# Optimization experiments

Hardware: AMD Instinct MI355X
Metric: run time of the kernel (lower is better)

## Reference

```python
import jax, jax.numpy as jnp
import numpy as np

CLIP = 50.0
EPS = 1e-8


def _attn_jacobian_agg(q, k, v, scale):
    """Aggregate attention Jacobian dO/dq summed over queries, plus attention outputs.

    q: (B, Q, d); k, v: (B, S, d).
    Per-query Jacobian: J_q = scale * sum_j p_j v_j (k_j - kbar)^T, kbar = sum_i p_i k_i.
    Returns (agg_jac: (B, d, d), outputs: (B, Q, d)).
    """
    scores = jnp.einsum('bqd,bsd->bqs', q, k) * scale
    p = jax.nn.softmax(scores, axis=-1)
    out = jnp.einsum('bqs,bsd->bqd', p, v)           # attention outputs O
    kbar = jnp.einsum('bqs,bsd->bqd', p, k)          # expected key per query
    # sum_j p_j v_j k_j^T  -> (B, Q, d, d)
    pvk = jnp.einsum('bqs,bsd,bse->bqde', p, v, k)
    jac = scale * (pvk - out[..., :, None] * kbar[..., None, :])
    return jac.sum(axis=1), out


def setup_inputs() -> dict:
    key = jax.random.key(0)
    ks = jax.random.split(key, 5)
    B, Q, S, M, D = 256, 16, 512, 8, 128
    return {
        'queries': jax.random.normal(ks[0], (B, Q, D), dtype=jnp.float32),
        'keys':    jax.random.normal(ks[1], (B, S, D), dtype=jnp.float32),
        'values':  jax.random.normal(ks[2], (B, S, D), dtype=jnp.float32),
        'k_cg':    jax.random.normal(ks[3], (B, M, D), dtype=jnp.float32),
        'v_cg':    jax.random.normal(ks[4], (B, M, D), dtype=jnp.float32),
    }


def reference(queries, keys, values, k_cg, v_cg):
    B, Q, d = queries.shape
    scale = d ** -0.5

    dense_jac, dense_out = _attn_jacobian_agg(queries, keys, values, scale)
    cg_jac, cg_out = _attn_jacobian_agg(queries, k_cg, v_cg, scale)

    # jacobian_clip_value = 50.0 (config default)
    dense_jac = jnp.clip(dense_jac, -CLIP, CLIP)
    cg_jac = jnp.clip(cg_jac, -CLIP, CLIP)

    df = dense_jac.reshape(B, -1)
    cf = cg_jac.reshape(B, -1)
    dn = jnp.linalg.norm(df, axis=-1)
    cn = jnp.linalg.norm(cf, axis=-1)
    cosine_sim = (df * cf).sum(axis=-1) / (dn * cn + EPS)
    force_direction_loss = 1.0 - cosine_sim

    # consistency: per-query output MSE, averaged over queries, scaled by 1/d_head
    out_diff = dense_out - cg_out
    per_query_mse = (out_diff ** 2).sum(axis=-1)          # (B, Q)
    consistency_loss = per_query_mse.sum(axis=-1) / Q / d  # (B,)

    # v4 loss: L = w_dir * L_force_cos + w_cons * L_consistency (defaults 1.0, 1.0)
    total = 1.0 * force_direction_loss + 1.0 * consistency_loss
    return total.mean()  # reduction='mean'
```

## Files before the change

kernel.cpp:

```cpp
#include <hip/hip_runtime.h>
#include <math.h>


namespace {
constexpr int Bn = 256, Qn = 16, Sn = 512, Mn = 8, Dn = 128;
constexpr int NT = 512;
constexpr float SCALE = 0.08838834764831845f;
constexpr float CLIPV = 50.0f;

constexpr int QS   = 0;
constexpr int PB   = 4352;
constexpr int WOFF = 20992;
constexpr int SMX0 = 23040;
constexpr int SMX1 = 23552;
constexpr int KT   = 24064;
constexpr int VT   = 34304;
constexpr int VTW  = 39424;
constexpr int CGS  = 44544;
constexpr int PCG  = 45056;
constexpr int WC   = 46336;
constexpr int RED  = 46368;
constexpr int LDSZ = 46496;

typedef __attribute__((ext_vector_type(8))) short bf16x8;
typedef __attribute__((ext_vector_type(4))) float f32x4;
#define MFMA16(a, b, c) __builtin_amdgcn_mfma_f32_16x16x32_bf16((a), (b), (c), 0, 0, 0)

__device__ inline unsigned int pack2t(float a, float b) {
  return __builtin_amdgcn_perm(__builtin_bit_cast(unsigned int, b),
                               __builtin_bit_cast(unsigned int, a), 0x07060302u);
}
__device__ inline unsigned short f2bf(float x) {
  unsigned int u = __builtin_bit_cast(unsigned int, x);
  u += 0x7fffu + ((u >> 16) & 1u);
  return (unsigned short)(u >> 16);
}
__device__ inline float bf2f(unsigned short h) {
  unsigned int u = ((unsigned int)h) << 16;
  return __builtin_bit_cast(float, u);
}
union Frag {
  bf16x8 v;
  unsigned int u[4];
  unsigned short h[8];
};

__global__ void zero_ws_kernel(float4* ws) {
  ws[threadIdx.x] = make_float4(0.f, 0.f, 0.f, 0.f);
}

__global__ void finalize_kernel(const float* __restrict__ ws, float* __restrict__ out) {
  __shared__ float sr[256];
  int i = threadIdx.x;
  float dt = ws[i * 4 + 0], n1 = ws[i * 4 + 1], n2 = ws[i * 4 + 2], cs = ws[i * 4 + 3];
  float cosv = dt / (sqrtf(n1) * sqrtf(n2) + 1e-8f);
  sr[i] = (1.0f - cosv) + cs * (1.0f / (float)(Qn * Dn));
  __syncthreads();
  for (int off = 128; off; off >>= 1) {
    if (i < off) sr[i] += sr[i + off];
    __syncthreads();
  }
  if (i == 0) out[0] = sr[0] * (1.0f / (float)Bn);
}

__global__ __launch_bounds__(NT, 6) void fm_kernel(
    const float* __restrict__ Qg, const float* __restrict__ Kg,
    const float* __restrict__ Vg, const float* __restrict__ Kcg,
    const float* __restrict__ Vcg, float* __restrict__ ws) {
  __shared__ __align__(16) char L[LDSZ];
  const int bid = blockIdx.x, b = bid >> 1, h = bid & 1;
  const int t = threadIdx.x, lane = t & 63, wv = t >> 6;
  const int quad = lane >> 4, l16 = lane & 15;

  const float* Qb = Qg + (size_t)b * Qn * Dn;
  const float* Kb = Kg + (size_t)b * Sn * Dn;
  const float* Vb = Vg + (size_t)b * Sn * Dn;
  const float* Kc = Kcg + (size_t)b * Mn * Dn;
  const float* Vc = Vcg + (size_t)b * Mn * Dn;

  const int dK = t & 127, gK = t >> 7;
  const int dV = t & 63, gV = (t >> 6) & 3;
  const bool vrole = t < 256;
  float kpf[8], vpf[8];

  auto load_tiles = [&](int st) {
    int s0 = st * 32 + gK * 8;
#pragma unroll
    for (int i = 0; i < 8; ++i) kpf[i] = Kb[(size_t)(s0 + i) * Dn + dK];
    if (vrole) {
      int s1 = st * 32 + gV * 8;
#pragma unroll
      for (int i = 0; i < 8; ++i) vpf[i] = Vb[(size_t)(s1 + i) * Dn + h * 64 + dV];
    }
  };
  auto store_tiles = [&](int st) {
    unsigned int u0 = pack2t(kpf[0], kpf[1]), u1 = pack2t(kpf[2], kpf[3]);
    unsigned int u2 = pack2t(kpf[4], kpf[5]), u3 = pack2t(kpf[6], kpf[7]);
    *(uint4*)(L + KT + dK * 80 + gK * 16) = make_uint4(u0, u1, u2, u3);
    if (vrole) {
      int s1 = st * 32 + gV * 8;
      float4 wlo = *(const float4*)(L + WOFF + s1 * 4);
      float4 whi = *(const float4*)(L + WOFF + s1 * 4 + 16);
      float wv8[8] = {wlo.x, wlo.y, wlo.z, wlo.w, whi.x, whi.y, whi.z, whi.w};
      unsigned int v0 = pack2t(vpf[0], vpf[1]), v1 = pack2t(vpf[2], vpf[3]);
      unsigned int v2 = pack2t(vpf[4], vpf[5]), v3 = pack2t(vpf[6], vpf[7]);
      *(uint4*)(L + VT + dV * 80 + gV * 16) = make_uint4(v0, v1, v2, v3);
      unsigned int w0 = pack2t(wv8[0] * vpf[0], wv8[1] * vpf[1]);
      unsigned int w1 = pack2t(wv8[2] * vpf[2], wv8[3] * vpf[3]);
      unsigned int w2 = pack2t(wv8[4] * vpf[4], wv8[5] * vpf[5]);
      unsigned int w3 = pack2t(wv8[6] * vpf[6], wv8[7] * vpf[7]);
      *(uint4*)(L + VTW + dV * 80 + gV * 16) = make_uint4(w0, w1, w2, w3);
    }
  };

  {
    int row = t >> 5, c4 = t & 31;
    float4 qv = ((const float4*)Qb)[t];
    unsigned int p0 = pack2t(qv.x * SCALE, qv.y * SCALE);
    unsigned int p1 = pack2t(qv.z * SCALE, qv.w * SCALE);
    *(unsigned long long*)(L + QS + row * 272 + c4 * 8) =
        (unsigned long long)p0 | ((unsigned long long)p1 << 32);
  }
  __syncthreads();

  float sc[4][4];
  {
    bf16x8 aq[4];
#pragma unroll
    for (int kk = 0; kk < 4; ++kk)
      aq[kk] = *(const bf16x8*)(L + QS + l16 * 272 + kk * 64 + quad * 16);
#pragma unroll
    for (int j = 0; j < 4; ++j) {
      const float* kp = Kb + (size_t)(64 * wv + 16 * j + l16) * Dn + quad * 8;
      f32x4 acc = {0.f, 0.f, 0.f, 0.f};
#pragma unroll
      for (int kk = 0; kk < 4; ++kk) {
        float4 lo = *(const float4*)(kp + kk * 32);
        float4 hi = *(const float4*)(kp + kk * 32 + 4);
        Frag f;
        f.u[0] = pack2t(lo.x, lo.y);
        f.u[1] = pack2t(lo.z, lo.w);
        f.u[2] = pack2t(hi.x, hi.y);
        f.u[3] = pack2t(hi.z, hi.w);
        acc = MFMA16(aq[kk], f.v, acc);
      }
#pragma unroll
      for (int r = 0; r < 4; ++r) sc[j][r] = acc[r];
    }
  }
  load_tiles(0);

  {
    float pm[4];
#pragma unroll
    for (int r = 0; r < 4; ++r)
      pm[r] = fmaxf(fmaxf(sc[0][r], sc[1][r]), fmaxf(sc[2][r], sc[3][r]));
#pragma unroll
    for (int o = 8; o; o >>= 1) {
#pragma unroll
      for (int r = 0; r < 4; ++r) pm[r] = fmaxf(pm[r], __shfl_xor(pm[r], o));
    }
    if (l16 == 0) {
#pragma unroll
      for (int r = 0; r < 4; ++r)
        *(float*)(L + SMX0 + ((quad * 4 + r) * 8 + wv) * 4) = pm[r];
    }
    __syncthreads();
    float gm[4];
#pragma unroll
    for (int r = 0; r < 4; ++r) {
      int q = quad * 4 + r;
      float4 a = *(const float4*)(L + SMX0 + q * 32);
      float4 c = *(const float4*)(L + SMX0 + q * 32 + 16);
      gm[r] = fmaxf(fmaxf(fmaxf(a.x, a.y), fmaxf(a.z, a.w)),
                    fmaxf(fmaxf(c.x, c.y), fmaxf(c.z, c.w)));
    }
    float ps[4] = {0.f, 0.f, 0.f, 0.f};
#pragma unroll
    for (int j = 0; j < 4; ++j) {
#pragma unroll
      for (int r = 0; r < 4; ++r) {
        sc[j][r] = __expf(sc[j][r] - gm[r]);
        ps[r] += sc[j][r];
      }
    }
#pragma unroll
    for (int o = 8; o; o >>= 1) {
#pragma unroll
      for (int r = 0; r < 4; ++r) ps[r] += __shfl_xor(ps[r], o);
    }
    if (l16 == 0) {
#pragma unroll
      for (int r = 0; r < 4; ++r)
        *(float*)(L + SMX1 + ((quad * 4 + r) * 8 + wv) * 4) = ps[r];
    }
    __syncthreads();
    float inv[4];
#pragma unroll
    for (int r = 0; r < 4; ++r) {
      int q = quad * 4 + r;
      float4 a = *(const float4*)(L + SMX1 + q * 32);
      float4 c = *(const float4*)(L + SMX1 + q * 32 + 16);
      inv[r] = 1.f / (a.x + a.y + a.z + a.w + c.x + c.y + c.z + c.w);
    }
#pragma unroll
    for (int j = 0; j < 4; ++j) {
      int s = 64 * wv + 16 * j + l16;
      float wpart = 0.f;
#pragma unroll
      for (int r = 0; r < 4; ++r) {
        float p = sc[j][r] * inv[r];
        *(unsigned short*)(L + PB + (quad * 4 + r) * 1040 + s * 2) = f2bf(p);
        wpart += p;
      }
      wpart += __shfl_xor(wpart, 16);
      wpart += __shfl_xor(wpart, 32);
      if (quad == j) *(float*)(L + WOFF + s * 4) = wpart;
    }
  }
  __syncthreads();

  const int rp = wv & 1, ch = wv >> 1;
  f32x4 C00 = {0.f,0.f,0.f,0.f}, C01 = {0.f,0.f,0.f,0.f};
  f32x4 C10 = {0.f,0.f,0.f,0.f}, C11 = {0.f,0.f,0.f,0.f};
  f32x4 outacc = {0.f,0.f,0.f,0.f}, kbacc = {0.f,0.f,0.f,0.f};

  auto ckstep = [&](f32x4& c00, f32x4& c01, f32x4& c10, f32x4& c11) {
    bf16x8 A0 = *(const bf16x8*)(L + VTW + (rp * 32 + l16) * 80 + quad * 16);
    bf16x8 A1 = *(const bf16x8*)(L + VTW + (rp * 32 + 16 + l16) * 80 + quad * 16);
    bf16x8 B0 = *(const bf16x8*)(L + KT + (ch * 32 + l16) * 80 + quad * 16);
    bf16x8 B1 = *(const bf16x8*)(L + KT + (ch * 32 + 16 + l16) * 80 + quad * 16);
    c00 = MFMA16(A0, B0, c00);
    c01 = MFMA16(A0, B1, c01);
    c10 = MFMA16(A1, B0, c10);
    c11 = MFMA16(A1, B1, c11);
  };

  for (int st = 0; st < 16; ++st) {
    if (st) __syncthreads();
    store_tiles(st);
    __syncthreads();
    if (st < 15) load_tiles(st + 1);
    bf16x8 pA = *(const bf16x8*)(L + PB + l16 * 1040 + st * 64 + quad * 16);
    bf16x8 bK = *(const bf16x8*)(L + KT + (wv * 16 + l16) * 80 + quad * 16);
    kbacc = MFMA16(pA, bK, kbacc);
    if (wv < 4) {
      bf16x8 bV = *(const bf16x8*)(L + VT + (wv * 16 + l16) * 80 + quad * 16);
      outacc = MFMA16(pA, bV, outacc);
    }
    ckstep(C00, C01, C10, C11);
  }
  __syncthreads();

  if (wv < 4) {
#pragma unroll
    for (int r = 0; r < 4; ++r)
      *(unsigned short*)(L + VTW + (wv * 16 + l16) * 80 + (quad * 4 + r) * 2) = f2bf(-outacc[r]);
  }
#pragma unroll
  for (int r = 0; r < 4; ++r)
    *(unsigned short*)(L + KT + (wv * 16 + l16) * 80 + (quad * 4 + r) * 2) = f2bf(kbacc[r]);
  if (t < 256) {
    *(uint4*)(L + KT + (t >> 1) * 80 + 32 + (t & 1) * 16) = make_uint4(0, 0, 0, 0);
  } else if (t < 384) {
    int i = t - 256;
    *(uint4*)(L + VTW + (i >> 1) * 80 + 32 + (i & 1) * 16) = make_uint4(0, 0, 0, 0);
  }
  __syncthreads();
  ckstep(C00, C01, C10, C11);
#pragma unroll
  for (int r = 0; r < 4; ++r) {
    C00[r] = fminf(fmaxf(SCALE * C00[r], -CLIPV), CLIPV);
    C01[r] = fminf(fmaxf(SCALE * C01[r], -CLIPV), CLIPV);
    C10[r] = fminf(fmaxf(SCALE * C10[r], -CLIPV), CLIPV);
    C11[r] = fminf(fmaxf(SCALE * C11[r], -CLIPV), CLIPV);
  }
  __syncthreads();

  if (wv == 0) {
    f32x4 acc = {0.f, 0.f, 0.f, 0.f};
    const float* kp = Kc + (size_t)(l16 & 7) * Dn + quad * 8;
#pragma unroll
    for (int kk = 0; kk < 4; ++kk) {
      bf16x8 a = *(const bf16x8*)(L + QS + l16 * 272 + kk * 64 + quad * 16);
      float4 lo = *(const float4*)(kp + kk * 32);
      float4 hi = *(const float4*)(kp + kk * 32 + 4);
      Frag f;
      f.u[0] = pack2t(lo.x, lo.y);
      f.u[1] = pack2t(lo.z, lo.w);
      f.u[2] = pack2t(hi.x, hi.y);
      f.u[3] = pack2t(hi.z, hi.w);
      acc = MFMA16(a, f.v, acc);
    }
    if (l16 < 8) {
#pragma unroll
      for (int r = 0; r < 4; ++r)
        *(float*)(L + CGS + (quad * 4 + r) * 32 + l16 * 4) = acc[r];
    }
  }
  __syncthreads();
  if (t < 16) {
    float xs[8];
    float m = -1e30f;
#pragma unroll
    for (int s = 0; s < 8; ++s) { xs[s] = *(const float*)(L + CGS + t * 32 + s * 4); m = fmaxf(m, xs[s]); }
    float ssum = 0.f;
#pragma unroll
    for (int s = 0; s < 8; ++s) { xs[s] = __expf(xs[s] - m); ssum += xs[s]; }
    float inv = 1.f / ssum;
#pragma unroll
    for (int s = 0; s < 4; ++s)
      *(unsigned int*)(L + PCG + t * 80 + s * 4) = pack2t(xs[2 * s] * inv, xs[2 * s + 1] * inv);
#pragma unroll
    for (int p = 4; p < 16; ++p) *(unsigned int*)(L + PCG + t * 80 + p * 4) = 0u;
  }
  __syncthreads();
  if (t < 8) {
    float s = 0.f;
#pragma unroll
    for (int q = 0; q < Qn; ++q) s += bf2f(*(const unsigned short*)(L + PCG + q * 80 + t * 2));
    *(float*)(L + WC + t * 4) = s;
  }
  __syncthreads();
  if (t < 128) {
    float kv[8];
#pragma unroll
    for (int i = 0; i < 8; ++i) kv[i] = Kc[(size_t)i * Dn + t];
    *(uint4*)(L + KT + t * 80) = make_uint4(pack2t(kv[0], kv[1]), pack2t(kv[2], kv[3]),
                                            pack2t(kv[4], kv[5]), pack2t(kv[6], kv[7]));
    *(uint4*)(L + KT + t * 80 + 16) = make_uint4(0, 0, 0, 0);
    *(uint4*)(L + KT + t * 80 + 32) = make_uint4(0, 0, 0, 0);
    *(uint4*)(L + KT + t * 80 + 48) = make_uint4(0, 0, 0, 0);
  } else if (t < 192) {
    int d = t - 128;
    float vv2[8];
#pragma unroll
    for (int i = 0; i < 8; ++i) vv2[i] = Vc[(size_t)i * Dn + h * 64 + d];
    *(uint4*)(L + VT + d * 80) = make_uint4(pack2t(vv2[0], vv2[1]), pack2t(vv2[2], vv2[3]),
                                            pack2t(vv2[4], vv2[5]), pack2t(vv2[6], vv2[7]));
    *(uint4*)(L + VT + d * 80 + 16) = make_uint4(0, 0, 0, 0);
    *(uint4*)(L + VT + d * 80 + 32) = make_uint4(0, 0, 0, 0);
    *(uint4*)(L + VT + d * 80 + 48) = make_uint4(0, 0, 0, 0);
  } else if (t < 256) {
    int d = t - 192;
    float vv2[8], wcv[8];
#pragma unroll
    for (int i = 0; i < 8; ++i) {
      vv2[i] = Vc[(size_t)i * Dn + h * 64 + d];
      wcv[i] = *(const float*)(L + WC + i * 4);
    }
    *(uint4*)(L + VTW + d * 80) =
        make_uint4(pack2t(wcv[0] * vv2[0], wcv[1] * vv2[1]), pack2t(wcv[2] * vv2[2], wcv[3] * vv2[3]),
                   pack2t(wcv[4] * vv2[4], wcv[5] * vv2[5]), pack2t(wcv[6] * vv2[6], wcv[7] * vv2[7]));
    *(uint4*)(L + VTW + d * 80 + 16) = make_uint4(0, 0, 0, 0);
    *(uint4*)(L + VTW + d * 80 + 32) = make_uint4(0, 0, 0, 0);
    *(uint4*)(L + VTW + d * 80 + 48) = make_uint4(0, 0, 0, 0);
  }
  __syncthreads();
  f32x4 outc = {0.f,0.f,0.f,0.f}, kbc = {0.f,0.f,0.f,0.f};
  f32x4 D00 = {0.f,0.f,0.f,0.f}, D01 = {0.f,0.f,0.f,0.f};
  f32x4 D10 = {0.f,0.f,0.f,0.f}, D11 = {0.f,0.f,0.f,0.f};
  {
    bf16x8 pA = *(const bf16x8*)(L + PCG + l16 * 80 + quad * 16);
    bf16x8 bK = *(const bf16x8*)(L + KT + (wv * 16 + l16) * 80 + quad * 16);
    kbc = MFMA16(pA, bK, kbc);
    if (wv < 4) {
      bf16x8 bV = *(const bf16x8*)(L + VT + (wv * 16 + l16) * 80 + quad * 16);
      outc = MFMA16(pA, bV, outc);
    }
    ckstep(D00, D01, D10, D11);
  }
  __syncthreads();
  if (wv < 4) {
#pragma unroll
    for (int r = 0; r < 4; ++r)
      *(unsigned short*)(L + VTW + (wv * 16 + l16) * 80 + (quad * 4 + r) * 2) = f2bf(-outc[r]);
  }
#pragma unroll
  for (int r = 0; r < 4; ++r)
    *(unsigned short*)(L + KT + (wv * 16 + l16) * 80 + (quad * 4 + r) * 2) = f2bf(kbc[r]);
  __syncthreads();
  ckstep(D00, D01, D10, D11);
#pragma unroll
  for (int r = 0; r < 4; ++r) {
    D00[r] = fminf(fmaxf(SCALE * D00[r], -CLIPV), CLIPV);
    D01[r] = fminf(fmaxf(SCALE * D01[r], -CLIPV), CLIPV);
    D10[r] = fminf(fmaxf(SCALE * D10[r], -CLIPV), CLIPV);
    D11[r] = fminf(fmaxf(SCALE * D11[r], -CLIPV), CLIPV);
  }

  float dot = 0.f, nd2 = 0.f, nc2 = 0.f, cons = 0.f;
#pragma unroll
  for (int r = 0; r < 4; ++r) {
    dot += C00[r] * D00[r] + C01[r] * D01[r] + C10[r] * D10[r] + C11[r] * D11[r];
    nd2 += C00[r] * C00[r] + C01[r] * C01[r] + C10[r] * C10[r] + C11[r] * C11[r];
    nc2 += D00[r] * D00[r] + D01[r] * D01[r] + D10[r] * D10[r] + D11[r] * D11[r];
  }
  if (wv < 4) {
#pragma unroll
    for (int r = 0; r < 4; ++r) {
      float df = outacc[r] - outc[r];
      cons += df * df;
    }
  }
#pragma unroll
  for (int o = 32; o; o >>= 1) {
    dot += __shfl_xor(dot, o);
    nd2 += __shfl_xor(nd2, o);
    nc2 += __shfl_xor(nc2, o);
    cons += __shfl_xor(cons, o);
  }
  if (lane == 0) {
    float* red = (float*)(L + RED);
    red[wv * 4 + 0] = dot;
    red[wv * 4 + 1] = nd2;
    red[wv * 4 + 2] = nc2;
    red[wv * 4 + 3] = cons;
  }
  __syncthreads();
  if (t == 0) {
    const float* red = (const float*)(L + RED);
    float d_ = 0.f, n1 = 0.f, n2 = 0.f, cs = 0.f;
#pragma unroll
    for (int w = 0; w < 8; ++w) {
      d_ += red[w * 4 + 0];
      n1 += red[w * 4 + 1];
      n2 += red[w * 4 + 2];
      cs += red[w * 4 + 3];
    }
    atomicAdd(ws + b * 4 + 0, d_);
    atomicAdd(ws + b * 4 + 1, n1);
    atomicAdd(ws + b * 4 + 2, n2);
    atomicAdd(ws + b * 4 + 3, cs);
  }
}
}

extern "C" void kernel_launch(void* const* d_in, const int* in_sizes, int n_in,
                              void* d_out, int out_size, void* d_ws, size_t ws_size,
                              hipStream_t stream) {
  const float* q = (const float*)d_in[0];
  const float* k = (const float*)d_in[1];
  const float* v = (const float*)d_in[2];
  const float* kc = (const float*)d_in[3];
  const float* vc = (const float*)d_in[4];
  float* out = (float*)d_out;
  float* ws = (float*)d_ws;
  zero_ws_kernel<<<1, 256, 0, stream>>>((float4*)ws);
  fm_kernel<<<2 * Bn, NT, 0, stream>>>(q, k, v, kc, vc, ws);
  finalize_kernel<<<1, 256, 0, stream>>>(ws, out);
}
```

Measured before the change: 181.2 us.

## Split each batch's Jacobian across four blocks by value and key halves

Each batch is now split into four blocks instead of two, each owning one half of the value dimension and one half of the key dimension of the d×d Jacobian. Per-block K tiles shrink to 64 columns, so the LDS footprint drops and the layout is repacked, and each wave now does two MFMAs per step instead of four. Launch bounds rise to 8 blocks per CU for more occupancy. In exchange, the softmax and score computation plus the Q load are repeated in twice as many blocks, and K and V rows are read from global memory by more blocks.

```diff
diff --git a/kernel.cpp b/kernel.cpp
--- a/kernel.cpp
+++ b/kernel.cpp
@@ -14,13 +14,13 @@
 constexpr int SMX0 = 23040;
 constexpr int SMX1 = 23552;
 constexpr int KT   = 24064;
-constexpr int VT   = 34304;
-constexpr int VTW  = 39424;
-constexpr int CGS  = 44544;
-constexpr int PCG  = 45056;
-constexpr int WC   = 46336;
-constexpr int RED  = 46368;
-constexpr int LDSZ = 46496;
+constexpr int VT   = 29184;
+constexpr int VTW  = 34304;
+constexpr int LDSZ = 39424;
+constexpr int CGS  = 20992;
+constexpr int PCG  = 21504;
+constexpr int WC   = 22784;
+constexpr int RED  = 22816;
 
 typedef __attribute__((ext_vector_type(8))) short bf16x8;
 typedef __attribute__((ext_vector_type(4))) float f32x4;
@@ -63,12 +63,13 @@
   if (i == 0) out[0] = sr[0] * (1.0f / (float)Bn);
 }
 
-__global__ __launch_bounds__(NT, 6) void fm_kernel(
+__global__ __launch_bounds__(NT, 8) void fm_kernel(
     const float* __restrict__ Qg, const float* __restrict__ Kg,
     const float* __restrict__ Vg, const float* __restrict__ Kcg,
     const float* __restrict__ Vcg, float* __restrict__ ws) {
   __shared__ __align__(16) char L[LDSZ];
-  const int bid = blockIdx.x, b = bid >> 1, h = bid & 1;
+  const int bid = blockIdx.x;
+  const int b = bid >> 2, hv = bid & 1, hk = (bid >> 1) & 1;
   const int t = threadIdx.x, lane = t & 63, wv = t >> 6;
   const int quad = lane >> 4, l16 = lane & 15;
 
@@ -78,38 +79,33 @@
   const float* Kc = Kcg + (size_t)b * Mn * Dn;
   const float* Vc = Vcg + (size_t)b * Mn * Dn;
 
-  const int dK = t & 127, gK = t >> 7;
-  const int dV = t & 63, gV = (t >> 6) & 3;
-  const bool vrole = t < 256;
-  float kpf[8], vpf[8];
+  const bool kRole = t < 256;
+  const int dS = t & 63, g8 = (t >> 6) & 3;
+  float pf[8];
 
   auto load_tiles = [&](int st) {
-    int s0 = st * 32 + gK * 8;
-#pragma unroll
-    for (int i = 0; i < 8; ++i) kpf[i] = Kb[(size_t)(s0 + i) * Dn + dK];
-    if (vrole) {
-      int s1 = st * 32 + gV * 8;
-#pragma unroll
-      for (int i = 0; i < 8; ++i) vpf[i] = Vb[(size_t)(s1 + i) * Dn + h * 64 + dV];
-    }
+    int s0 = st * 32 + g8 * 8;
+    const float* base = kRole ? (Kb + (size_t)s0 * Dn + hk * 64 + dS)
+                              : (Vb + (size_t)s0 * Dn + hv * 64 + dS);
+#pragma unroll
+    for (int i = 0; i < 8; ++i) pf[i] = base[(size_t)i * Dn];
   };
   auto store_tiles = [&](int st) {
-    unsigned int u0 = pack2t(kpf[0], kpf[1]), u1 = pack2t(kpf[2], kpf[3]);
-    unsigned int u2 = pack2t(kpf[4], kpf[5]), u3 = pack2t(kpf[6], kpf[7]);
-    *(uint4*)(L + KT + dK * 80 + gK * 16) = make_uint4(u0, u1, u2, u3);
-    if (vrole) {
-      int s1 = st * 32 + gV * 8;
+    if (kRole) {
+      *(uint4*)(L + KT + dS * 80 + g8 * 16) =
+          make_uint4(pack2t(pf[0], pf[1]), pack2t(pf[2], pf[3]),
+                     pack2t(pf[4], pf[5]), pack2t(pf[6], pf[7]));
+    } else {
+      int s1 = st * 32 + g8 * 8;
       float4 wlo = *(const float4*)(L + WOFF + s1 * 4);
       float4 whi = *(const float4*)(L + WOFF + s1 * 4 + 16);
-      float wv8[8] = {wlo.x, wlo.y, wlo.z, wlo.w, whi.x, whi.y, whi.z, whi.w};
-      unsigned int v0 = pack2t(vpf[0], vpf[1]), v1 = pack2t(vpf[2], vpf[3]);
-      unsigned int v2 = pack2t(vpf[4], vpf[5]), v3 = pack2t(vpf[6], vpf[7]);
-      *(uint4*)(L + VT + dV * 80 + gV * 16) = make_uint4(v0, v1, v2, v3);
-      unsigned int w0 = pack2t(wv8[0] * vpf[0], wv8[1] * vpf[1]);
-      unsigned int w1 = pack2t(wv8[2] * vpf[2], wv8[3] * vpf[3]);
-      unsigned int w2 = pack2t(wv8[4] * vpf[4], wv8[5] * vpf[5]);
-      unsigned int w3 = pack2t(wv8[6] * vpf[6], wv8[7] * vpf[7]);
-      *(uint4*)(L + VTW + dV * 80 + gV * 16) = make_uint4(w0, w1, w2, w3);
+      float w8[8] = {wlo.x, wlo.y, wlo.z, wlo.w, whi.x, whi.y, whi.z, whi.w};
+      *(uint4*)(L + VT + dS * 80 + g8 * 16) =
+          make_uint4(pack2t(pf[0], pf[1]), pack2t(pf[2], pf[3]),
+                     pack2t(pf[4], pf[5]), pack2t(pf[6], pf[7]));
+      *(uint4*)(L + VTW + dS * 80 + g8 * 16) =
+          make_uint4(pack2t(w8[0] * pf[0], w8[1] * pf[1]), pack2t(w8[2] * pf[2], w8[3] * pf[3]),
+                     pack2t(w8[4] * pf[4], w8[5] * pf[5]), pack2t(w8[6] * pf[6], w8[7] * pf[7]));
     }
   };
 
@@ -220,20 +216,17 @@
   }
   __syncthreads();
 
-  const int rp = wv & 1, ch = wv >> 1;
-  f32x4 C00 = {0.f,0.f,0.f,0.f}, C01 = {0.f,0.f,0.f,0.f};
-  f32x4 C10 = {0.f,0.f,0.f,0.f}, C11 = {0.f,0.f,0.f,0.f};
-  f32x4 outacc = {0.f,0.f,0.f,0.f}, kbacc = {0.f,0.f,0.f,0.f};
-
-  auto ckstep = [&](f32x4& c00, f32x4& c01, f32x4& c10, f32x4& c11) {
-    bf16x8 A0 = *(const bf16x8*)(L + VTW + (rp * 32 + l16) * 80 + quad * 16);
-    bf16x8 A1 = *(const bf16x8*)(L + VTW + (rp * 32 + 16 + l16) * 80 + quad * 16);
-    bf16x8 B0 = *(const bf16x8*)(L + KT + (ch * 32 + l16) * 80 + quad * 16);
-    bf16x8 B1 = *(const bf16x8*)(L + KT + (ch * 32 + 16 + l16) * 80 + quad * 16);
-    c00 = MFMA16(A0, B0, c00);
-    c01 = MFMA16(A0, B1, c01);
-    c10 = MFMA16(A1, B0, c10);
-    c11 = MFMA16(A1, B1, c11);
+  const int rp = wv & 3, chn = wv >> 2;
+  f32x4 c0 = {0.f,0.f,0.f,0.f}, c1 = {0.f,0.f,0.f,0.f};
+  f32x4 okacc = {0.f,0.f,0.f,0.f};
+  const char* okBase = (wv < 4) ? (L + VT) : (L + KT);
+
+  auto ckstep = [&](f32x4& a0, f32x4& a1) {
+    bf16x8 A0 = *(const bf16x8*)(L + VTW + (rp * 16 + l16) * 80 + quad * 16);
+    bf16x8 B0 = *(const bf16x8*)(L + KT + (chn * 32 + l16) * 80 + quad * 16);
+    bf16x8 B1 = *(const bf16x8*)(L + KT + (chn * 32 + 16 + l16) * 80 + quad * 16);
+    a0 = MFMA16(A0, B0, a0);
+    a1 = MFMA16(A0, B1, a1);
   };
 
   for (int st = 0; st < 16; ++st) {
@@ -242,38 +235,33 @@
     __syncthreads();
     if (st < 15) load_tiles(st + 1);
     bf16x8 pA = *(const bf16x8*)(L + PB + l16 * 1040 + st * 64 + quad * 16);
-    bf16x8 bK = *(const bf16x8*)(L + KT + (wv * 16 + l16) * 80 + quad * 16);
-    kbacc = MFMA16(pA, bK, kbacc);
-    if (wv < 4) {
-      bf16x8 bV = *(const bf16x8*)(L + VT + (wv * 16 + l16) * 80 + quad * 16);
-      outacc = MFMA16(pA, bV, outacc);
-    }
-    ckstep(C00, C01, C10, C11);
+    bf16x8 bOK = *(const bf16x8*)(okBase + ((wv & 3) * 16 + l16) * 80 + quad * 16);
+    okacc = MFMA16(pA, bOK, okacc);
+    ckstep(c0, c1);
   }
   __syncthreads();
 
   if (wv < 4) {
 #pragma unroll
     for (int r = 0; r < 4; ++r)
-      *(unsigned short*)(L + VTW + (wv * 16 + l16) * 80 + (quad * 4 + r) * 2) = f2bf(-outacc[r]);
-  }
-#pragma unroll
-  for (int r = 0; r < 4; ++r)
-    *(unsigned short*)(L + KT + (wv * 16 + l16) * 80 + (quad * 4 + r) * 2) = f2bf(kbacc[r]);
-  if (t < 256) {
+      *(unsigned short*)(L + VTW + (wv * 16 + l16) * 80 + (quad * 4 + r) * 2) = f2bf(-okacc[r]);
+  } else {
+#pragma unroll
+    for (int r = 0; r < 4; ++r)
+      *(unsigned short*)(L + KT + ((wv - 4) * 16 + l16) * 80 + (quad * 4 + r) * 2) = f2bf(okacc[r]);
+  }
+  if (t < 128) {
     *(uint4*)(L + KT + (t >> 1) * 80 + 32 + (t & 1) * 16) = make_uint4(0, 0, 0, 0);
-  } else if (t < 384) {
-    int i = t - 256;
+  } else if (t < 256) {
+    int i = t - 128;
     *(uint4*)(L + VTW + (i >> 1) * 80 + 32 + (i & 1) * 16) = make_uint4(0, 0, 0, 0);
   }
   __syncthreads();
-  ckstep(C00, C01, C10, C11);
+  ckstep(c0, c1);
 #pragma unroll
   for (int r = 0; r < 4; ++r) {
-    C00[r] = fminf(fmaxf(SCALE * C00[r], -CLIPV), CLIPV);
-    C01[r] = fminf(fmaxf(SCALE * C01[r], -CLIPV), CLIPV);
-    C10[r] = fminf(fmaxf(SCALE * C10[r], -CLIPV), CLIPV);
-    C11[r] = fminf(fmaxf(SCALE * C11[r], -CLIPV), CLIPV);
+    c0[r] = fminf(fmaxf(SCALE * c0[r], -CLIPV), CLIPV);
+    c1[r] = fminf(fmaxf(SCALE * c1[r], -CLIPV), CLIPV);
   }
   __syncthreads();
 
@@ -322,31 +310,31 @@
     *(float*)(L + WC + t * 4) = s;
   }
   __syncthreads();
-  if (t < 128) {
+  if (t < 64) {
     float kv[8];
 #pragma unroll
-    for (int i = 0; i < 8; ++i) kv[i] = Kc[(size_t)i * Dn + t];
+    for (int i = 0; i < 8; ++i) kv[i] = Kc[(size_t)i * Dn + hk * 64 + t];
     *(uint4*)(L + KT + t * 80) = make_uint4(pack2t(kv[0], kv[1]), pack2t(kv[2], kv[3]),
                                             pack2t(kv[4], kv[5]), pack2t(kv[6], kv[7]));
     *(uint4*)(L + KT + t * 80 + 16) = make_uint4(0, 0, 0, 0);
     *(uint4*)(L + KT + t * 80 + 32) = make_uint4(0, 0, 0, 0);
     *(uint4*)(L + KT + t * 80 + 48) = make_uint4(0, 0, 0, 0);
-  } else if (t < 192) {
-    int d = t - 128;
+  } else if (t < 128) {
+    int d = t - 64;
     float vv2[8];
 #pragma unroll
-    for (int i = 0; i < 8; ++i) vv2[i] = Vc[(size_t)i * Dn + h * 64 + d];
+    for (int i = 0; i < 8; ++i) vv2[i] = Vc[(size_t)i * Dn + hv * 64 + d];
     *(uint4*)(L + VT + d * 80) = make_uint4(pack2t(vv2[0], vv2[1]), pack2t(vv2[2], vv2[3]),
                                             pack2t(vv2[4], vv2[5]), pack2t(vv2[6], vv2[7]));
     *(uint4*)(L + VT + d * 80 + 16) = make_uint4(0, 0, 0, 0);
     *(uint4*)(L + VT + d * 80 + 32) = make_uint4(0, 0, 0, 0);
     *(uint4*)(L + VT + d * 80 + 48) = make_uint4(0, 0, 0, 0);
-  } else if (t < 256) {
-    int d = t - 192;
+  } else if (t < 192) {
+    int d = t - 128;
     float vv2[8], wcv[8];
 #pragma unroll
     for (int i = 0; i < 8; ++i) {
-      vv2[i] = Vc[(size_t)i * Dn + h * 64 + d];
+      vv2[i] = Vc[(size_t)i * Dn + hv * 64 + d];
       wcv[i] = *(const float*)(L + WC + i * 4);
     }
     *(uint4*)(L + VTW + d * 80) =
@@ -357,49 +345,43 @@
     *(uint4*)(L + VTW + d * 80 + 48) = make_uint4(0, 0, 0, 0);
   }
   __syncthreads();
-  f32x4 outc = {0.f,0.f,0.f,0.f}, kbc = {0.f,0.f,0.f,0.f};
-  f32x4 D00 = {0.f,0.f,0.f,0.f}, D01 = {0.f,0.f,0.f,0.f};
-  f32x4 D10 = {0.f,0.f,0.f,0.f}, D11 = {0.f,0.f,0.f,0.f};
+  f32x4 d0 = {0.f,0.f,0.f,0.f}, d1 = {0.f,0.f,0.f,0.f};
+  f32x4 okc = {0.f,0.f,0.f,0.f};
   {
     bf16x8 pA = *(const bf16x8*)(L + PCG + l16 * 80 + quad * 16);
-    bf16x8 bK = *(const bf16x8*)(L + KT + (wv * 16 + l16) * 80 + quad * 16);
-    kbc = MFMA16(pA, bK, kbc);
-    if (wv < 4) {
-      bf16x8 bV = *(const bf16x8*)(L + VT + (wv * 16 + l16) * 80 + quad * 16);
-      outc = MFMA16(pA, bV, outc);
-    }
-    ckstep(D00, D01, D10, D11);
+    bf16x8 bOK = *(const bf16x8*)(okBase + ((wv & 3) * 16 + l16) * 80 + quad * 16);
+    okc = MFMA16(pA, bOK, okc);
+    ckstep(d0, d1);
   }
   __syncthreads();
   if (wv < 4) {
 #pragma unroll
     for (int r = 0; r < 4; ++r)
-      *(unsigned short*)(L + VTW + (wv * 16 + l16) * 80 + (quad * 4 + r) * 2) = f2bf(-outc[r]);
-  }
-#pragma unroll
-  for (int r = 0; r < 4; ++r)
-    *(unsigned short*)(L + KT + (wv * 16 + l16) * 80 + (quad * 4 + r) * 2) = f2bf(kbc[r]);
-  __syncthreads();
-  ckstep(D00, D01, D10, D11);
+      *(unsigned short*)(L + VTW + (wv * 16 + l16) * 80 + (quad * 4 + r) * 2) = f2bf(-okc[r]);
+  } else {
+#pragma unroll
+    for (int r = 0; r < 4; ++r)
+      *(unsigned short*)(L + KT + ((wv - 4) * 16 + l16) * 80 + (quad * 4 + r) * 2) = f2bf(okc[r]);
+  }
+  __syncthreads();
+  ckstep(d0, d1);
 #pragma unroll
   for (int r = 0; r < 4; ++r) {
-    D00[r] = fminf(fmaxf(SCALE * D00[r], -CLIPV), CLIPV);
-    D01[r] = fminf(fmaxf(SCALE * D01[r], -CLIPV), CLIPV);
-    D10[r] = fminf(fmaxf(SCALE * D10[r], -CLIPV), CLIPV);
-    D11[r] = fminf(fmaxf(SCALE * D11[r], -CLIPV), CLIPV);
+    d0[r] = fminf(fmaxf(SCALE * d0[r], -CLIPV), CLIPV);
+    d1[r] = fminf(fmaxf(SCALE * d1[r], -CLIPV), CLIPV);
   }
 
   float dot = 0.f, nd2 = 0.f, nc2 = 0.f, cons = 0.f;
 #pragma unroll
   for (int r = 0; r < 4; ++r) {
-    dot += C00[r] * D00[r] + C01[r] * D01[r] + C10[r] * D10[r] + C11[r] * D11[r];
-    nd2 += C00[r] * C00[r] + C01[r] * C01[r] + C10[r] * C10[r] + C11[r] * C11[r];
-    nc2 += D00[r] * D00[r] + D01[r] * D01[r] + D10[r] * D10[r] + D11[r] * D11[r];
-  }
-  if (wv < 4) {
+    dot += c0[r] * d0[r] + c1[r] * d1[r];
+    nd2 += c0[r] * c0[r] + c1[r] * c1[r];
+    nc2 += d0[r] * d0[r] + d1[r] * d1[r];
+  }
+  if (hk == 0 && wv < 4) {
 #pragma unroll
     for (int r = 0; r < 4; ++r) {
-      float df = outacc[r] - outc[r];
+      float df = okacc[r] - okc[r];
       cons += df * df;
     }
   }
@@ -447,6 +429,6 @@
   float* out = (float*)d_out;
   float* ws = (float*)d_ws;
   zero_ws_kernel<<<1, 256, 0, stream>>>((float4*)ws);
-  fm_kernel<<<2 * Bn, NT, 0, stream>>>(q, k, v, kc, vc, ws);
+  fm_kernel<<<4 * Bn, NT, 0, stream>>>(q, k, v, kc, vc, ws);
   finalize_kernel<<<1, 256, 0, stream>>>(ws, out);
 }
```

Measured after the change: 199.7 us. +10.2%, slower.
